# Performance work log

Measured on AMD Instinct MI355X. Metric: run time of the kernel, lower is better.

The kernel has to match this reference:

```python
import jax, jax.numpy as jnp
import numpy as np

T, B, IN, H, L = 300, 32, 320, 1024, 3  # seq, batch, input, hidden, layers (bidirectional)


def _init_params(key):
    stdv = 1.0 / np.sqrt(H)
    ks = jax.random.split(key, 8)
    u = lambda k, shp: jax.random.uniform(k, shp, jnp.float32, -stdv, stdv)
    # layer 0 (input IN), 2 directions
    w_ih0 = u(ks[0], (2, 4 * H, IN))
    w_hh0 = u(ks[1], (2, 4 * H, H))
    b_ih0 = u(ks[2], (2, 4 * H))
    b_hh0 = u(ks[3], (2, 4 * H))
    # layers 1..L-1 (input 2H), 2 directions
    w_ihL = u(ks[4], (L - 1, 2, 4 * H, 2 * H))
    w_hhL = u(ks[5], (L - 1, 2, 4 * H, H))
    b_ihL = u(ks[6], (L - 1, 2, 4 * H))
    b_hhL = u(ks[7], (L - 1, 2, 4 * H))
    # forget_gate_bias = 1.0 applied to bias_ih[H:2H], bias_hh[H:2H] = 0
    fgb = 1.0
    b_ih0 = b_ih0.at[:, H:2 * H].set(fgb)
    b_hh0 = b_hh0.at[:, H:2 * H].set(0.0)
    b_ihL = b_ihL.at[:, :, H:2 * H].set(fgb)
    b_hhL = b_hhL.at[:, :, H:2 * H].set(0.0)
    return dict(w_ih0=w_ih0, w_hh0=w_hh0, b_ih0=b_ih0, b_hh0=b_hh0,
                w_ihL=w_ihL, w_hhL=w_hhL, b_ihL=b_ihL, b_hhL=b_hhL)


def setup_inputs() -> dict:
    key = jax.random.key(0)
    k1, k2 = jax.random.split(key)
    inp = {
        "x": jax.random.normal(k1, (T, B, IN), jnp.float32),
        "h0": jnp.zeros((L * 2, B, H), jnp.float32),
        "c0": jnp.zeros((L * 2, B, H), jnp.float32),
    }
    inp.update(_init_params(k2))
    return inp


def _hard_sigmoid(z):
    return jnp.clip(0.2 * z + 0.5, 0.0, 1.0)


def _lstm_dir(x_seq, w_ih, w_hh, b_ih, b_hh, h0, c0, reverse):
    # x_seq: [T, B, D_in]; returns ys [T,B,H], (h,c) [B,H]
    xs = jnp.flip(x_seq, 0) if reverse else x_seq
    gx = jnp.einsum('tbi,gi->tbg', xs, w_ih) + b_ih + b_hh  # [T,B,4H]

    def step(carry, gxt):
        h, c = carry
        gates = gxt + h @ w_hh.T
        i, f, g, o = jnp.split(gates, 4, axis=-1)
        i = _hard_sigmoid(i)
        f = _hard_sigmoid(f)
        g = jnp.clip(g, -1.0, 1.0)  # hardtanh
        o = _hard_sigmoid(o)
        c = f * c + i * g
        h = o * jnp.clip(c, -1.0, 1.0)
        return (h, c), h

    (h, c), ys = jax.lax.scan(step, (h0, c0), gx)
    if reverse:
        ys = jnp.flip(ys, 0)
    return ys, h, c


def _stacked_forward(x, h0, c0, w_ih0, w_hh0, b_ih0, b_hh0, w_ihL, w_hhL, b_ihL, b_hhL):
    # Faithful to StackedLSTM: hn = hx[0].view(L,2,B,H); cn = hn (source bug: cell
    # init comes from h0, c0 ignored). h0/c0 are zeros so this is also correct math.
    hn = h0.reshape(L, 2, B, H)
    cn = hn
    out = x
    hs, cs = [], []
    for l in range(L):
        if l == 0:
            wih, whh, bih, bhh = w_ih0, w_hh0, b_ih0, b_hh0
        else:
            wih, whh, bih, bhh = w_ihL[l - 1], w_hhL[l - 1], b_ihL[l - 1], b_hhL[l - 1]
        yf, hf, cf = _lstm_dir(out, wih[0], whh[0], bih[0], bhh[0], hn[l, 0], cn[l, 0], False)
        yb, hb, cb = _lstm_dir(out, wih[1], whh[1], bih[1], bhh[1], hn[l, 1], cn[l, 1], True)
        out = jnp.concatenate([yf, yb], axis=-1)  # [T,B,2H]
        hs += [hf, hb]
        cs += [cf, cb]
    hn_out = jnp.stack(hs)  # [L*2, B, H]
    cn_out = jnp.stack(cs)
    return out, hn_out, cn_out


def reference(x, h0, c0, w_ih0, w_hh0, b_ih0, b_hh0, w_ihL, w_hhL, b_ihL, b_hhL):
    return _stacked_forward(x, h0, c0, w_ih0, w_hh0, b_ih0, b_hh0,
                            w_ihL, w_hhL, b_ihL, b_hhL)
```

## Files before the change

### kernel.cpp

```cpp
#include <hip/hip_runtime.h>

typedef __bf16 bf16;
typedef __attribute__((ext_vector_type(8))) __bf16 bf16x8;
typedef __attribute__((ext_vector_type(4))) float f32x4;

#define GLOBAL_AS __attribute__((address_space(1)))
#define LDS_AS __attribute__((address_space(3)))

__device__ __forceinline__ void gload_lds16(const void* g, void* l) {
  __builtin_amdgcn_global_load_lds((const GLOBAL_AS void*)g, (LDS_AS void*)l, 16, 0, 0);
}
__device__ __forceinline__ void gload_lds16_cc(const void* g, void* l) {
  __builtin_amdgcn_global_load_lds((const GLOBAL_AS void*)g, (LDS_AS void*)l, 16, 0, 0x11);
}

__device__ __forceinline__ f32x4 mfma16(bf16x8 a, bf16x8 b, f32x4 c) {
  return __builtin_amdgcn_mfma_f32_16x16x32_bf16(a, b, c, 0, 0, 0);
}

#define T_SEQ 300
#define NBATCH 32
#define DIN 320
#define NH 1024
#define NG 4096
#define MROWS 9600
#define OUT_Y 19660800
#define HN_SZ 196608

__global__ __launch_bounds__(256) void k_cvt(const float* __restrict__ src,
                                             bf16* __restrict__ dst, int n8) {
  int stride = gridDim.x * blockDim.x;
  for (int i = blockIdx.x * blockDim.x + threadIdx.x; i < n8; i += stride) {
    const float* s = src + (size_t)i * 8;
    f32x4 a = *(const f32x4*)s;
    f32x4 b = *(const f32x4*)(s + 4);
    bf16x8 o;
#pragma unroll
    for (int j = 0; j < 4; ++j) { o[j] = (bf16)a[j]; o[j + 4] = (bf16)b[j]; }
    *(bf16x8*)(dst + (size_t)i * 8) = o;
  }
}

__global__ __launch_bounds__(256) void k_bsum(const float* __restrict__ bih0,
                                              const float* __restrict__ bhh0,
                                              const float* __restrict__ bihL,
                                              const float* __restrict__ bhhL,
                                              float* __restrict__ bsum) {
  int i = blockIdx.x * 256 + threadIdx.x;
  if (i < 2 * NG) bsum[i] = bih0[i] + bhh0[i];
  else            bsum[i] = bihL[i - 2 * NG] + bhhL[i - 2 * NG];
}

__global__ __launch_bounds__(256) void k_gemm_gx(const bf16* __restrict__ A,
                                                 const bf16* __restrict__ Bw,
                                                 const float* __restrict__ bias,
                                                 bf16* __restrict__ gxout, int K) {
  __shared__ bf16 As[128 * 32];
  __shared__ bf16 Bs[128 * 32];
  const int t = threadIdx.x;
  const int m0 = blockIdx.y * 128, n0 = blockIdx.x * 128;
  const int lane = t & 63, wid = t >> 6;
  const int wr = wid >> 1, wc = wid & 1;
  const int fr = lane & 15, fq = lane >> 4;
  f32x4 acc[4][4] = {};
  for (int k0 = 0; k0 < K; k0 += 32) {
#pragma unroll
    for (int r = 0; r < 2; ++r) {
      int idx = r * 256 + t;
      int row = idx >> 2, kk = (idx & 3) * 8;
      gload_lds16(A + (size_t)(m0 + row) * K + k0 + kk, As + (size_t)idx * 8);
      gload_lds16(Bw + (size_t)(n0 + row) * K + k0 + kk, Bs + (size_t)idx * 8);
    }
    asm volatile("s_waitcnt vmcnt(0)" ::: "memory");
    __syncthreads();
    bf16x8 af[4], bf_[4];
#pragma unroll
    for (int i2 = 0; i2 < 4; ++i2) {
      af[i2]  = *(const bf16x8*)(As + (wr * 64 + i2 * 16 + fr) * 32 + fq * 8);
      bf_[i2] = *(const bf16x8*)(Bs + (wc * 64 + i2 * 16 + fr) * 32 + fq * 8);
    }
#pragma unroll
    for (int mi = 0; mi < 4; ++mi)
#pragma unroll
      for (int ni = 0; ni < 4; ++ni)
        acc[mi][ni] = mfma16(af[mi], bf_[ni], acc[mi][ni]);
    __syncthreads();
  }
#pragma unroll
  for (int ni = 0; ni < 4; ++ni) {
    int col = n0 + wc * 64 + ni * 16 + fr;
    float bv = bias[col];
    int dir = col >> 12, grow = col & (NG - 1);
    int gg = grow >> 10, uu = grow & 1023;
    bf16* base = gxout + ((size_t)dir * 300 * 4 + gg) * 32768 + uu;
#pragma unroll
    for (int mi = 0; mi < 4; ++mi) {
#pragma unroll
      for (int j = 0; j < 4; ++j) {
        int row = m0 + wr * 64 + mi * 16 + fq * 4 + j;
        int tt = row >> 5, b = row & 31;
        base[(size_t)tt * 131072 + b * 1024] = (bf16)(acc[mi][ni][j] + bv);
      }
    }
  }
}

__global__ __launch_bounds__(256) void k_init(const float* __restrict__ h0,
                                              bf16* __restrict__ hbuf,
                                              int* __restrict__ flags, int layer) {
  int i = blockIdx.x * 256 + threadIdx.x;
  hbuf[i] = (bf16)h0[(size_t)layer * 65536 + i];
  if (blockIdx.x == 0 && threadIdx.x < 64) flags[threadIdx.x] = 0;
}

__global__ __launch_bounds__(512, 1) void k_rec(
    const bf16* __restrict__ whh,
    const bf16* __restrict__ gxT,
    const float* __restrict__ h0,
    bf16* __restrict__ hbuf,
    int* __restrict__ flags,
    bf16* __restrict__ yout,
    float* __restrict__ dout,
    int layer,
    const bf16* __restrict__ gB,
    const float* __restrict__ gbias,
    int ngemm) {
  __shared__ char smem_[98304];
  float* EX = (float*)smem_;
  char* GXL = smem_ + 67584;

  const int tid = threadIdx.x;
  const int bid = blockIdx.x;

  if (bid >= 64) {
    const int gid = bid - 64;
    if (gid >= ngemm) return;
    const int lane = tid & 63, wid = tid >> 6;
    const int wr = wid >> 2, wc = wid & 3;
    const int fr = lane & 15, fq = lane >> 4;
    const int strow = tid >> 2, stkk = (tid & 3) * 8;
#pragma unroll 1
    for (int i = 0; i < 25; ++i) {
      const int lin = i * 192 + gid;
      const int n0 = (lin & 63) << 7;
      const int mrank = lin >> 6;
      const int m = (mrank & 1) ? (37 - ((mrank + 1) >> 1)) : (37 + (mrank >> 1));
      const int m0 = m << 7;
      const int ra = 4 * m + 3, rb = 299 - 4 * m;
      const int thr = (ra > rb ? ra : rb) + 2;
      if (tid < 64) {
        while (__hip_atomic_load(&flags[tid], __ATOMIC_RELAXED,
                                 __HIP_MEMORY_SCOPE_AGENT) < thr)
          __builtin_amdgcn_s_sleep(32);
      }
      __syncthreads();
      __builtin_amdgcn_fence(__ATOMIC_ACQUIRE, "agent");

      const bf16* Arow = yout + (size_t)(m0 + strow) * 2048 + stkk;
      const bf16* Brow = gB + (size_t)(n0 + strow) * 2048 + stkk;
      const int ldst = (strow * 32 + stkk) * 2;

      auto stage = [&](int ks) {
        char* buf = smem_ + (ks % 6) * 16384;
        gload_lds16(Arow + ks * 32, buf + ldst);
        gload_lds16(Brow + ks * 32, buf + 8192 + ldst);
      };

      f32x4 acc[4][2] = {};
      auto compute = [&](int k) {
        const bf16* As = (const bf16*)(smem_ + (k % 6) * 16384);
        const bf16* Bs = As + 4096;
        bf16x8 af[4], bfv[2];
#pragma unroll
        for (int i2 = 0; i2 < 4; ++i2)
          af[i2] = *(const bf16x8*)(As + (wr * 64 + i2 * 16 + fr) * 32 + fq * 8);
#pragma unroll
        for (int i2 = 0; i2 < 2; ++i2)
          bfv[i2] = *(const bf16x8*)(Bs + (wc * 32 + i2 * 16 + fr) * 32 + fq * 8);
#pragma unroll
        for (int mi = 0; mi < 4; ++mi)
#pragma unroll
          for (int ni = 0; ni < 2; ++ni)
            acc[mi][ni] = mfma16(af[mi], bfv[ni], acc[mi][ni]);
      };

#pragma unroll
      for (int s = 0; s < 6; ++s) stage(s);

#pragma unroll 1
      for (int k = 0; k < 59; ++k) {
        asm volatile("s_waitcnt vmcnt(10)" ::: "memory");
        __builtin_amdgcn_s_barrier();
        compute(k);
        __builtin_amdgcn_sched_barrier(0);
        __builtin_amdgcn_s_barrier();
        if (k + 6 < 64) stage(k + 6);
      }
#define GTAIL(K, WAITS)                                          \
      asm volatile("s_waitcnt vmcnt(" WAITS ")" ::: "memory");   \
      __builtin_amdgcn_s_barrier();                              \
      compute(K);                                                \
      __builtin_amdgcn_sched_barrier(0);                         \
      __builtin_amdgcn_s_barrier();
      GTAIL(59, "8") GTAIL(60, "6") GTAIL(61, "4") GTAIL(62, "2") GTAIL(63, "0")
#undef GTAIL

#pragma unroll
      for (int ni = 0; ni < 2; ++ni) {
        int col = n0 + wc * 32 + ni * 16 + fr;
        float bv = gbias[col];
        int dirv = col >> 12, grow = col & (NG - 1);
        int gg = grow >> 10, uu = grow & 1023;
        bf16* base = (bf16*)gxT + ((size_t)dirv * 1200 + gg) * 32768 + uu;
#pragma unroll
        for (int mi = 0; mi < 4; ++mi) {
#pragma unroll
          for (int j = 0; j < 4; ++j) {
            int row = m0 + wr * 64 + mi * 16 + fq * 4 + j;
            int tt = row >> 5, b = row & 31;
            base[(size_t)tt * 131072 + b * 1024] = (bf16)(acc[mi][ni][j] + bv);
          }
        }
      }
    }
    return;
  }

  const int dir = bid >> 5;
  const int rank = bid & 31;
  const int u0 = rank << 5;
  const int w = tid >> 6, lane = tid & 63;
  const int fr = lane & 15, fq = lane >> 4;
  const int kh = w >> 1, rh = w & 1;

  f32x4 wf[32];
#pragma unroll
  for (int rg = 0; rg < 4; ++rg) {
    int rowb = rh * 64 + rg * 16 + fr;
    const bf16* Wp = whh + ((size_t)dir * 4096 + (rowb >> 5) * 1024 + u0 + (rowb & 31)) * 1024
                     + kh * 256 + fq * 8;
#pragma unroll
    for (int it = 0; it < 8; ++it) wf[rg * 8 + it] = *(const f32x4*)(Wp + it * 32);
  }
#pragma unroll
  for (int i = 0; i < 32; ++i) asm volatile("" : "+v"(wf[i]));

  const int b_pt = tid >> 4;
  const int ul_pt = (tid & 15) << 1;
  const int ug_pt = u0 + ul_pt;
  const size_t soff = ((size_t)layer * 2 + dir) * 32768 + (size_t)b_pt * 1024 + ug_pt;
  float c0 = h0[soff], c1 = h0[soff + 1];
  float hl0 = 0.f, hl1 = 0.f;

  const int gg = tid >> 7, sub = tid & 127;
  const size_t gx_base0 = ((size_t)dir * 1200 + gg) * 32768
                          + (size_t)(sub >> 2) * 1024 + u0 + (sub & 3) * 8;

  int srcoff[8];
#pragma unroll
  for (int r = 0; r < 8; ++r) {
    int d = r * 8192 + tid * 16;
    int row = d >> 11, colb = d & 2047;
    srcoff[r] = row * 2048 + (colb ^ ((row & 7) << 4));
  }
  const int swz = (fr & 7) << 4;

  {
    const int ts0 = dir ? (T_SEQ - 1) : 0;
    gload_lds16(gxT + gx_base0 + (size_t)ts0 * 131072, GXL + tid * 16);
  }

#pragma unroll 1
  for (int t = 0; t < T_SEQ; ++t) {
    const int tseq = dir ? (T_SEQ - 1 - t) : t;

    if (tid < 32) {
      while (__hip_atomic_load(&flags[dir * 32 + tid], __ATOMIC_RELAXED,
                               __HIP_MEMORY_SCOPE_AGENT) < t)
        __builtin_amdgcn_s_sleep(1);
    }
    __syncthreads();

    const char* hsrc = (const char*)hbuf + (((size_t)(t & 1) * 2 + dir) << 16);
#pragma unroll
    for (int r = 0; r < 8; ++r)
      gload_lds16_cc(hsrc + srcoff[r], smem_ + r * 8192 + tid * 16);
    asm volatile("s_waitcnt vmcnt(0)" ::: "memory");
    __syncthreads();

    f32x4 acc[4][2] = {};
    const char* hb0 = smem_ + fr * 2048;
#pragma unroll
    for (int it = 0; it < 8; ++it) {
      int col = kh * 512 + it * 64 + fq * 16;
      bf16x8 ha0 = *(const bf16x8*)(hb0 + (col ^ swz));
      bf16x8 ha1 = *(const bf16x8*)(hb0 + 32768 + (col ^ swz));
#pragma unroll
      for (int rg = 0; rg < 4; ++rg) {
        bf16x8 wv = __builtin_bit_cast(bf16x8, wf[rg * 8 + it]);
        acc[rg][0] = mfma16(ha0, wv, acc[rg][0]);
        acc[rg][1] = mfma16(ha1, wv, acc[rg][1]);
      }
    }
    __syncthreads();

#pragma unroll
    for (int rg = 0; rg < 4; ++rg) {
      int rowb = rh * 64 + rg * 16 + fr;
      float* exr = EX + (size_t)(kh * 128 + rowb) * 33;
#pragma unroll
      for (int j = 0; j < 4; ++j) {
        exr[fq * 4 + j]      = acc[rg][0][j];
        exr[16 + fq * 4 + j] = acc[rg][1][j];
      }
    }
    __syncthreads();

    const bf16* gxb = (const bf16*)(GXL + (t & 1) * 8192);
    float hv[2]; float cc[2] = {c0, c1};
#pragma unroll
    for (int q = 0; q < 2; ++q) {
      int ul = ul_pt + q;
      float gt[4];
#pragma unroll
      for (int g2 = 0; g2 < 4; ++g2) {
        int rowb = g2 * 32 + ul;
        float s = EX[(size_t)(0 * 128 + rowb) * 33 + b_pt]
                + EX[(size_t)(1 * 128 + rowb) * 33 + b_pt]
                + EX[(size_t)(2 * 128 + rowb) * 33 + b_pt]
                + EX[(size_t)(3 * 128 + rowb) * 33 + b_pt];
        gt[g2] = s + (float)gxb[(g2 * 32 + b_pt) * 32 + ul];
      }
      float iv = fminf(fmaxf(__builtin_fmaf(0.2f, gt[0], 0.5f), 0.f), 1.f);
      float fv = fminf(fmaxf(__builtin_fmaf(0.2f, gt[1], 0.5f), 0.f), 1.f);
      float gv = fminf(fmaxf(gt[2], -1.f), 1.f);
      float ov = fminf(fmaxf(__builtin_fmaf(0.2f, gt[3], 0.5f), 0.f), 1.f);
      float c = fv * cc[q] + iv * gv;
      cc[q] = c;
      hv[q] = ov * fminf(fmaxf(c, -1.f), 1.f);
    }
    c0 = cc[0]; c1 = cc[1]; hl0 = hv[0]; hl1 = hv[1];

    unsigned hp;
    { union { bf16 h[2]; unsigned u; } pk; pk.h[0] = (bf16)hv[0]; pk.h[1] = (bf16)hv[1]; hp = pk.u; }
    volatile unsigned* hdst =
        (volatile unsigned*)((char*)hbuf + (((size_t)((t + 1) & 1) * 2 + dir) << 16))
        + (((size_t)b_pt * 1024 + ug_pt) >> 1);
    *hdst = hp;
    asm volatile("s_waitcnt vmcnt(0)" ::: "memory");
    __syncthreads();
    if (tid == 0)
      __hip_atomic_store(&flags[bid], t + 1, __ATOMIC_RELAXED, __HIP_MEMORY_SCOPE_AGENT);

    if (yout) {
      volatile unsigned* yd =
          (volatile unsigned*)((char*)yout
              + (((size_t)tseq * 32 + b_pt) * 2048 + dir * 1024 + ug_pt) * 2);
      *yd = hp;
    } else {
      float* yd = dout + ((size_t)tseq * 32 + b_pt) * 2048 + dir * 1024 + ug_pt;
      yd[0] = hv[0]; yd[1] = hv[1];
    }
    if (t + 1 < T_SEQ) {
      const int tn = dir ? (T_SEQ - 2 - t) : (t + 1);
      gload_lds16(gxT + gx_base0 + (size_t)tn * 131072,
                  GXL + ((t + 1) & 1) * 8192 + tid * 16);
    }
  }

  dout[OUT_Y + soff] = hl0;
  dout[OUT_Y + soff + 1] = hl1;
  dout[OUT_Y + HN_SZ + soff] = c0;
  dout[OUT_Y + HN_SZ + soff + 1] = c1;
  asm volatile("s_waitcnt vmcnt(0)" ::: "memory");
  __syncthreads();
  if (tid == 0)
    __hip_atomic_store(&flags[bid], 302, __ATOMIC_RELAXED, __HIP_MEMORY_SCOPE_AGENT);
}

extern "C" void kernel_launch(void* const* d_in, const int* in_sizes, int n_in,
                              void* d_out, int out_size, void* d_ws, size_t ws_size,
                              hipStream_t stream) {
  const float* x     = (const float*)d_in[0];
  const float* h0    = (const float*)d_in[1];
  const float* w_ih0 = (const float*)d_in[3];
  const float* w_hh0 = (const float*)d_in[4];
  const float* b_ih0 = (const float*)d_in[5];
  const float* b_hh0 = (const float*)d_in[6];
  const float* w_ihL = (const float*)d_in[7];
  const float* w_hhL = (const float*)d_in[8];
  const float* b_ihL = (const float*)d_in[9];
  const float* b_hhL = (const float*)d_in[10];
  float* dout = (float*)d_out;
  char* ws = (char*)d_ws;

  const size_t OFF_XB   = 0;
  const size_t OFF_WIH0 = 6144000;
  const size_t OFF_WIHL = 11386880;
  const size_t OFF_WHH  = 78495744;
  const size_t OFF_BSUM = 128827392;
  const size_t OFF_GX   = 128925696;
  const size_t OFF_Y0   = 286212096;
  const size_t OFF_Y1   = 325533696;
  const size_t OFF_HBF  = 364855296;
  const size_t OFF_FLG  = 365117440;

  bf16*  xb    = (bf16*)(ws + OFF_XB);
  bf16*  wih0b = (bf16*)(ws + OFF_WIH0);
  bf16*  wihLb = (bf16*)(ws + OFF_WIHL);
  bf16*  whhb  = (bf16*)(ws + OFF_WHH);
  float* bsum  = (float*)(ws + OFF_BSUM);
  bf16*  gx    = (bf16*)(ws + OFF_GX);
  bf16*  y0    = (bf16*)(ws + OFF_Y0);
  bf16*  y1    = (bf16*)(ws + OFF_Y1);
  bf16*  hbuf  = (bf16*)(ws + OFF_HBF);
  int*   flags = (int*)(ws + OFF_FLG);

  auto cvt = [&](const float* s, bf16* d, size_t n) {
    int n8 = (int)(n / 8);
    int grid = (n8 + 255) / 256; if (grid > 2048) grid = 2048;
    k_cvt<<<grid, 256, 0, stream>>>(s, d, n8);
  };

  cvt(x,     xb,    (size_t)MROWS * DIN);
  cvt(w_ih0, wih0b, (size_t)2 * NG * DIN);
  cvt(w_ihL, wihLb, (size_t)2 * 2 * NG * 2048);
  cvt(w_hh0, whhb,  (size_t)2 * NG * NH);
  cvt(w_hhL, whhb + (size_t)2 * NG * NH, (size_t)4 * NG * NH);
  k_bsum<<<96, 256, 0, stream>>>(b_ih0, b_hh0, b_ihL, b_hhL, bsum);

  k_gemm_gx<<<dim3(64, 75), 256, 0, stream>>>(xb, wih0b, bsum, gx, DIN);

  for (int l = 0; l < 3; ++l) {
    k_init<<<256, 256, 0, stream>>>(h0, hbuf, flags, l);

    const bf16* whh_l = whhb + (size_t)l * 2 * NG * NH;
    bf16* yout = (l == 0) ? y0 : (l == 1 ? y1 : nullptr);
    const int ngemm = (l < 2) ? 192 : 0;
    const bf16* gB = wihLb + (size_t)l * 2 * NG * 2048;
    const float* gbias = bsum + (size_t)(l + 1) * 2 * NG;
    k_rec<<<64 + ngemm, 512, 0, stream>>>(whh_l, gx, h0, hbuf, flags, yout, dout, l,
                                          gB, gbias, ngemm);
  }
  (void)in_sizes; (void)n_in; (void)out_size; (void)ws_size;
}
```

Before: 4.753 ms.

## Enlarge input-projection GEMM tiles to 256x256 with triple-buffered LDS staging

The gx input-projection GEMM, run by the extra blocks alongside the recurrent blocks, moves from 128x128 tiles with a 6-deep LDS pipeline to 256x256 tiles with a 3-deep pipeline. Each wave now computes 64x128 outputs using 32 accumulators, which raises arithmetic intensity and cuts global/LDS traffic per flop. It also changes the tile-to-timestep ordering and readiness thresholds and adds a row bound check because 9600 rows do not divide evenly. The cost is much higher register pressure, coarser dependency granularity on the recurrent progress flags, and fewer tiles to balance across the 192 blocks.

Result: no change. 4.714 ms (-0.8%).

```diff
diff --git a/kernel.cpp b/kernel.cpp
--- a/kernel.cpp
+++ b/kernel.cpp
@@ -17,6 +17,8 @@
 __device__ __forceinline__ f32x4 mfma16(bf16x8 a, bf16x8 b, f32x4 c) {
   return __builtin_amdgcn_mfma_f32_16x16x32_bf16(a, b, c, 0, 0, 0);
 }
+
+#define GBAR() asm volatile("s_barrier" ::: "memory")
 
 #define T_SEQ 300
 #define NBATCH 32
@@ -136,17 +138,21 @@
     const int gid = bid - 64;
     if (gid >= ngemm) return;
     const int lane = tid & 63, wid = tid >> 6;
-    const int wr = wid >> 2, wc = wid & 3;
+    const int wm = wid >> 1, wn = wid & 1;
     const int fr = lane & 15, fq = lane >> 4;
-    const int strow = tid >> 2, stkk = (tid & 3) * 8;
+    const int srow = tid >> 2;
+    const int scol = (tid & 3) * 8;
+    const int l16 = tid * 16;
 #pragma unroll 1
-    for (int i = 0; i < 25; ++i) {
+    for (int i = 0; i < 7; ++i) {
       const int lin = i * 192 + gid;
-      const int n0 = (lin & 63) << 7;
-      const int mrank = lin >> 6;
-      const int m = (mrank & 1) ? (37 - ((mrank + 1) >> 1)) : (37 + (mrank >> 1));
-      const int m0 = m << 7;
-      const int ra = 4 * m + 3, rb = 299 - 4 * m;
+      if (lin >= 1216) break;
+      const int n0 = (lin & 31) << 8;
+      const int mrank = lin >> 5;
+      const int m = (mrank & 1) ? (19 + (mrank >> 1)) : (18 - (mrank >> 1));
+      const int m0 = m << 8;
+      int ra = 8 * m + 7; if (ra > 299) ra = 299;
+      const int rb = 299 - 8 * m;
       const int thr = (ra > rb ? ra : rb) + 2;
       if (tid < 64) {
         while (__hip_atomic_load(&flags[tid], __ATOMIC_RELAXED,
@@ -156,58 +162,62 @@
       __syncthreads();
       __builtin_amdgcn_fence(__ATOMIC_ACQUIRE, "agent");
 
-      const bf16* Arow = yout + (size_t)(m0 + strow) * 2048 + stkk;
-      const bf16* Brow = gB + (size_t)(n0 + strow) * 2048 + stkk;
-      const int ldst = (strow * 32 + stkk) * 2;
+      const bf16* ArowL = yout + (size_t)(m0 + srow) * 2048 + scol;
+      const bf16* ArowH = yout + (size_t)(m0 + 128 + srow) * 2048 + scol;
+      const bf16* BrowL = gB + (size_t)(n0 + srow) * 2048 + scol;
+      const bf16* BrowH = gB + (size_t)(n0 + 128 + srow) * 2048 + scol;
 
       auto stage = [&](int ks) {
-        char* buf = smem_ + (ks % 6) * 16384;
-        gload_lds16(Arow + ks * 32, buf + ldst);
-        gload_lds16(Brow + ks * 32, buf + 8192 + ldst);
+        char* buf = smem_ + (ks % 3) * 32768;
+        gload_lds16(ArowL + ks * 32, buf + l16);
+        gload_lds16(ArowH + ks * 32, buf + 8192 + l16);
+        gload_lds16(BrowL + ks * 32, buf + 16384 + l16);
+        gload_lds16(BrowH + ks * 32, buf + 24576 + l16);
       };
 
-      f32x4 acc[4][2] = {};
+      f32x4 acc[4][8] = {};
       auto compute = [&](int k) {
-        const bf16* As = (const bf16*)(smem_ + (k % 6) * 16384);
-        const bf16* Bs = As + 4096;
-        bf16x8 af[4], bfv[2];
+        const bf16* As = (const bf16*)(smem_ + (k % 3) * 32768);
+        const bf16* Bs = As + 8192;
+        bf16x8 af[4], bfv[8];
 #pragma unroll
         for (int i2 = 0; i2 < 4; ++i2)
-          af[i2] = *(const bf16x8*)(As + (wr * 64 + i2 * 16 + fr) * 32 + fq * 8);
-#pragma unroll
-        for (int i2 = 0; i2 < 2; ++i2)
-          bfv[i2] = *(const bf16x8*)(Bs + (wc * 32 + i2 * 16 + fr) * 32 + fq * 8);
+          af[i2] = *(const bf16x8*)(As + (wm * 64 + i2 * 16 + fr) * 32 + fq * 8);
+#pragma unroll
+        for (int i2 = 0; i2 < 8; ++i2)
+          bfv[i2] = *(const bf16x8*)(Bs + (wn * 128 + i2 * 16 + fr) * 32 + fq * 8);
 #pragma unroll
         for (int mi = 0; mi < 4; ++mi)
 #pragma unroll
-          for (int ni = 0; ni < 2; ++ni)
+          for (int ni = 0; ni < 8; ++ni)
             acc[mi][ni] = mfma16(af[mi], bfv[ni], acc[mi][ni]);
       };
 
-#pragma unroll
-      for (int s = 0; s < 6; ++s) stage(s);
+      stage(0); stage(1); stage(2);
 
 #pragma unroll 1
-      for (int k = 0; k < 59; ++k) {
-        asm volatile("s_waitcnt vmcnt(10)" ::: "memory");
-        __builtin_amdgcn_s_barrier();
+      for (int k = 0; k < 61; ++k) {
+        asm volatile("s_waitcnt vmcnt(8)" ::: "memory");
+        GBAR();
+        __builtin_amdgcn_sched_barrier(0);
         compute(k);
         __builtin_amdgcn_sched_barrier(0);
-        __builtin_amdgcn_s_barrier();
-        if (k + 6 < 64) stage(k + 6);
+        GBAR();
+        stage(k + 3);
       }
 #define GTAIL(K, WAITS)                                          \
       asm volatile("s_waitcnt vmcnt(" WAITS ")" ::: "memory");   \
-      __builtin_amdgcn_s_barrier();                              \
+      GBAR();                                                    \
+      __builtin_amdgcn_sched_barrier(0);                         \
       compute(K);                                                \
       __builtin_amdgcn_sched_barrier(0);                         \
-      __builtin_amdgcn_s_barrier();
-      GTAIL(59, "8") GTAIL(60, "6") GTAIL(61, "4") GTAIL(62, "2") GTAIL(63, "0")
+      GBAR();
+      GTAIL(61, "8") GTAIL(62, "4") GTAIL(63, "0")
 #undef GTAIL
 
 #pragma unroll
-      for (int ni = 0; ni < 2; ++ni) {
-        int col = n0 + wc * 32 + ni * 16 + fr;
+      for (int ni = 0; ni < 8; ++ni) {
+        int col = n0 + wn * 128 + ni * 16 + fr;
         float bv = gbias[col];
         int dirv = col >> 12, grow = col & (NG - 1);
         int gg = grow >> 10, uu = grow & 1023;
@@ -216,9 +226,11 @@
         for (int mi = 0; mi < 4; ++mi) {
 #pragma unroll
           for (int j = 0; j < 4; ++j) {
-            int row = m0 + wr * 64 + mi * 16 + fq * 4 + j;
-            int tt = row >> 5, b = row & 31;
-            base[(size_t)tt * 131072 + b * 1024] = (bf16)(acc[mi][ni][j] + bv);
+            int row = m0 + wm * 64 + mi * 16 + fq * 4 + j;
+            if (row < MROWS) {
+              int tt = row >> 5, b = row & 31;
+              base[(size_t)tt * 131072 + b * 1024] = (bf16)(acc[mi][ni][j] + bv);
+            }
           }
         }
       }
```
